# Kernel tuning notes

Measured on AMD Instinct MI355X. Metric: run time of the kernel, lower is better.

## Reference

```python
import jax, jax.numpy as jnp
import numpy as np

C = 256; GC = 32; G = C // GC; K = 3; S = 1; NEW = 2; PAD = (K - 1) // 2
IN1 = C * K * 2 + C * K * K // 32          # 1608
OUT1 = G * NEW * NEW * K * K // 4          # 72
OUT2 = G * NEW * NEW * K * K               # 288
B = 8; H = 56; W = 56


def setup_inputs():
    key = jax.random.key(0)
    k0, k1, k2 = jax.random.split(key, 3)
    inputs = jax.random.normal(k0, (B, C, H, W), jnp.float32)
    W1 = jax.random.normal(k1, (OUT1, IN1), jnp.float32) * np.float32(1.0 / np.sqrt(IN1))
    b1 = jnp.zeros((OUT1,), jnp.float32)
    W2 = jax.random.normal(k2, (OUT2, OUT1), jnp.float32) * np.float32(1.0 / np.sqrt(OUT1))
    b2 = jnp.zeros((OUT2,), jnp.float32)
    return {"inputs": inputs, "W1": W1, "b1": b1, "W2": W2, "b2": b2}


def _unfold(x, h, w):
    # torch.nn.Unfold(K, 1, PAD, S): patches of shape (B, C, K, K, h, w)
    xp = jnp.pad(x, ((0, 0), (0, 0), (PAD, PAD), (PAD, PAD)))
    cols = [xp[:, :, di:di + (h - 1) * S + 1:S, dj:dj + (w - 1) * S + 1:S]
            for di in range(K) for dj in range(K)]  # fixed K*K=9 slices
    return jnp.stack(cols, axis=2).reshape(x.shape[0], x.shape[1], K, K, h, w)


def reference(inputs, W1, b1, W2, b2):
    b, c, Hh, Ww = inputs.shape
    h = (Hh + 2 * PAD - K) // S + 1
    w = (Ww + 2 * PAD - K) // S + 1
    # (B, G, GC, K, K, h, w)
    x = _unfold(inputs, h, w).reshape(b, G, GC, K, K, h, w)
    # three max-pooled descriptors over different axes
    x1 = x.reshape(b, G, -1, GC // 32, K, K, h, w).max(axis=2).reshape(b, -1, h, w)  # (B, C*K*K//32, h, w)
    x2 = x.max(axis=3).reshape(b, -1, h, w)  # (B, C*K, h, w)
    x3 = x.max(axis=4).reshape(b, -1, h, w)  # (B, C*K, h, w)
    feat = jnp.concatenate([x1, x2, x3], axis=1)  # (B, IN1, h, w)
    # two biased 1x1 convs (ConvModule with no norm/act)
    y = jnp.einsum('bchw,oc->bohw', feat, W1) + b1[None, :, None, None]
    y = jnp.einsum('bchw,oc->bohw', y, W2) + b2[None, :, None, None]
    # softmax over the K*K kernel-window dim
    wgt = jax.nn.softmax(y.reshape(b, G, K * K, NEW * NEW, h, w), axis=2)
    # softmax-weighted local aggregation: sum over kernel window
    agg = jnp.einsum('bgckhw,bgknhw->bgcnhw', x.reshape(b, G, GC, K * K, h, w), wgt)
    # fold with non-overlapping (NEW, NEW) blocks == block upsampling reshape
    return agg.reshape(b, C, NEW, NEW, h, w).transpose(0, 1, 4, 2, 5, 3).reshape(b, C, h * NEW, w * NEW)
```

## Files before the change

kernel.cpp:

```cpp
#include <hip/hip_runtime.h>

#define CC   256
#define HH   56
#define WWID 56
#define KIN1 1608
#define KP1  1632
#define NO1  72
#define NO2  288
#define PPB  14
#define H2   112
#define W2D  112

typedef unsigned short u16;
typedef unsigned int   u32;
typedef __attribute__((ext_vector_type(8))) short v8s;
typedef __attribute__((ext_vector_type(4))) float v4f;
typedef __attribute__((ext_vector_type(4))) unsigned short us4;

#define W1BF_ELEMS (80 * KP1)
#define W2BF_OFF_B 262144

#define LDS_TOTAL 35840
#define OFF_A 0
#define OFF_B 21504
#define OFF_C 29696
#define OFF_D 32768

#define SWZ(row) (((row) & 7) << 3)

__device__ __forceinline__ u16 f2b(float x) {
  u32 u = __float_as_uint(x);
  u = (u + 0x7FFFu + ((u >> 16) & 1u)) >> 16;
  return (u16)u;
}

__global__ void kConvW(const float* __restrict__ W1, const float* __restrict__ W2,
                       u16* __restrict__ w1bf, u16* __restrict__ w2bf) {
  int idx = blockIdx.x * 256 + threadIdx.x;
  if (idx < W1BF_ELEMS) {
    int m = idx / KP1, k = idx - m * KP1;
    float v = 0.f;
    if (m < NO1) {
      int orig = -1;
      if (k < 768)                 orig = 72 + (k & 255) * 3 + (k >> 8);
      else if (k < 1536)           orig = 840 + (k & 255) * 3 + ((k - 768) >> 8);
      else if ((k - 1536) < NO1)   orig = k - 1536;
      if (orig >= 0) v = W1[m * KIN1 + orig];
    }
    w1bf[idx] = f2b(v);
  } else {
    int i2 = idx - W1BF_ELEMS;
    if (i2 < NO2 * 96) {
      int m = i2 / 96, k = i2 - m * 96;
      w2bf[i2] = (k < NO1) ? f2b(W2[m * NO1 + k]) : (u16)0;
    }
  }
}

__global__ __launch_bounds__(256, 4)
void kFused(const float* __restrict__ in, const u16* __restrict__ w1bf,
            const float* __restrict__ b1, const u16* __restrict__ w2bf,
            const float* __restrict__ b2, float* __restrict__ out) {
  __shared__ __align__(16) char lds[LDS_TOTAL];
  u16*   rowmaxT = (u16*)(lds + OFF_A);
  u16*   colmaxT = (u16*)(lds + OFF_B);
  u16*   x1T     = (u16*)(lds + OFF_C);
  u16*   y1b     = (u16*)(lds + OFF_D);
  float* y2L     = (float*)(lds + OFF_A);

  const int t  = threadIdx.x;
  const int L  = blockIdx.x + 4 * (blockIdx.y + 56 * blockIdx.z);
  const int jq = L >> 3;
  const int jt = jq & 3, i = jq >> 2, b = L & 7;
  const int c  = t;
  const int g  = c >> 5;
  const int gc = c & 31;
  const int w  = t >> 6, lane = t & 63;
  const int ml = lane & 15, quad = lane >> 4;

  {
    u32* xu = (u32*)x1T;
    u32* yu = (u32*)y1b;
    if (t < 132) {
#pragma unroll
      for (int rp2 = 0; rp2 < 2; ++rp2) {
        int idx = 2 * t + rp2;
        int off;
        if (idx < 192) {
          int row = idx / 12;
          off = (row * 48 + 36 + (idx - row * 12)) ^ ((row & 7) << 2);
        } else {
          int e = idx - 192, row = 14 + e / 36;
          off = (row * 48 + (e % 36)) ^ ((row & 7) << 2);
        }
        xu[off] = 0u;
        yu[off] = 0u;
      }
    }
  }

  const float* rowbase0 = in + ((size_t)b * CC + c) * (HH * WWID);
  u32 win_p[3][8];
  float colmax[16];
#pragma unroll
  for (int k = 0; k < 16; ++k) colmax[k] = -3.0e38f;

#pragma unroll
  for (int r = 0; r < 3; ++r) {
    const int row = i - 1 + r;
    float sc[16];
    if (row < 0 || row >= HH) {
#pragma unroll
      for (int k = 0; k < 16; ++k) sc[k] = 0.f;
    } else {
      const float* rp = rowbase0 + row * WWID;
      float l[20];
      if (jt == 0) {
        const float4 a0 = *(const float4*)(rp), a1 = *(const float4*)(rp + 4),
                     a2 = *(const float4*)(rp + 8), a3 = *(const float4*)(rp + 12);
        l[0]=a0.x;l[1]=a0.y;l[2]=a0.z;l[3]=a0.w; l[4]=a1.x;l[5]=a1.y;l[6]=a1.z;l[7]=a1.w;
        l[8]=a2.x;l[9]=a2.y;l[10]=a2.z;l[11]=a2.w; l[12]=a3.x;l[13]=a3.y;l[14]=a3.z;l[15]=a3.w;
        sc[0] = 0.f;
#pragma unroll
        for (int k = 1; k < 16; ++k) sc[k] = l[k - 1];
      } else if (jt == 3) {
        const float* q = rp + 40;
        const float4 a0 = *(const float4*)(q), a1 = *(const float4*)(q + 4),
                     a2 = *(const float4*)(q + 8), a3 = *(const float4*)(q + 12);
        l[0]=a0.x;l[1]=a0.y;l[2]=a0.z;l[3]=a0.w; l[4]=a1.x;l[5]=a1.y;l[6]=a1.z;l[7]=a1.w;
        l[8]=a2.x;l[9]=a2.y;l[10]=a2.z;l[11]=a2.w; l[12]=a3.x;l[13]=a3.y;l[14]=a3.z;l[15]=a3.w;
#pragma unroll
        for (int k = 0; k < 15; ++k) sc[k] = l[k + 1];
        sc[15] = 0.f;
      } else {
        const float* q = rp + ((jt == 1) ? 12 : 24);
        const float4 a0 = *(const float4*)(q), a1 = *(const float4*)(q + 4),
                     a2 = *(const float4*)(q + 8), a3 = *(const float4*)(q + 12),
                     a4 = *(const float4*)(q + 16);
        l[0]=a0.x;l[1]=a0.y;l[2]=a0.z;l[3]=a0.w; l[4]=a1.x;l[5]=a1.y;l[6]=a1.z;l[7]=a1.w;
        l[8]=a2.x;l[9]=a2.y;l[10]=a2.z;l[11]=a2.w; l[12]=a3.x;l[13]=a3.y;l[14]=a3.z;l[15]=a3.w;
        l[16]=a4.x;l[17]=a4.y;l[18]=a4.z;l[19]=a4.w;
        if (jt == 1) {
#pragma unroll
          for (int k = 0; k < 16; ++k) sc[k] = l[k + 1];
        } else {
#pragma unroll
          for (int k = 0; k < 16; ++k) sc[k] = l[k + 3];
        }
      }
    }
#pragma unroll
    for (int k = 0; k < 16; ++k) colmax[k] = fmaxf(colmax[k], sc[k]);
#pragma unroll
    for (int n = 0; n < 14; ++n)
      rowmaxT[(n * 768 + r * 256 + c) ^ SWZ(n)] =
          f2b(fmaxf(fmaxf(sc[n], sc[n + 1]), sc[n + 2]));
#pragma unroll
    for (int col = 0; col < 16; ++col) {
      float m = sc[col];
      m = fmaxf(m, __shfl_xor(m, 1));
      m = fmaxf(m, __shfl_xor(m, 2));
      m = fmaxf(m, __shfl_xor(m, 4));
      m = fmaxf(m, __shfl_xor(m, 8));
      m = fmaxf(m, __shfl_xor(m, 16));
      if (gc == col) {
        u16 mv = f2b(m);
#pragma unroll
        for (int kj = 0; kj < 3; ++kj) {
          const int n = col - kj;
          if (n >= 0 && n < 14)
            x1T[(n * 96 + g * 9 + r * 3 + kj) ^ SWZ(n)] = mv;
        }
      }
    }
#pragma unroll
    for (int k = 0; k < 8; ++k)
      win_p[r][k] = (u32)f2b(sc[2 * k]) | ((u32)f2b(sc[2 * k + 1]) << 16);
  }
#pragma unroll
  for (int col = 0; col < 16; ++col)
    colmaxT[(col * 256 + c) ^ SWZ(col)] = f2b(colmax[col]);
  __syncthreads();

  auto loadB = [&](int ks) -> v8s {
    if (ks < 24) {
      int kj = ks >> 3, c0 = (ks & 7) * 32, rowi = ml + kj;
      return *(v8s*)&colmaxT[(rowi * 256 + c0 + quad * 8) ^ SWZ(rowi)];
    } else if (ks < 48) {
      return *(v8s*)&rowmaxT[(ml * 768 + (ks - 24) * 32 + quad * 8) ^ SWZ(ml)];
    } else {
      return *(v8s*)&x1T[(ml * 96 + (ks - 48) * 32 + quad * 8) ^ SWZ(ml)];
    }
  };

  {
    v4f acc0 = (v4f){0.f, 0.f, 0.f, 0.f};
    const u16* ap0 = w1bf + (w * 16 + ml) * KP1 + quad * 8;
    if (w == 0) {
      v4f acc1 = (v4f){0.f, 0.f, 0.f, 0.f};
      const u16* ap1 = w1bf + (64 + ml) * KP1 + quad * 8;
#pragma unroll
      for (int ks = 0; ks < 51; ++ks) {
        v8s bf = loadB(ks);
        v8s a0 = *(const v8s*)(ap0 + ks * 32);
        v8s a1 = *(const v8s*)(ap1 + ks * 32);
        acc0 = __builtin_amdgcn_mfma_f32_16x16x32_bf16(a0, bf, acc0, 0, 0, 0);
        acc1 = __builtin_amdgcn_mfma_f32_16x16x32_bf16(a1, bf, acc1, 0, 0, 0);
      }
      if (ml < 14) {
        const float4 bv0 = *(const float4*)(b1 + quad * 4);
        us4 h0;
        h0.x = f2b(acc0[0] + bv0.x); h0.y = f2b(acc0[1] + bv0.y);
        h0.z = f2b(acc0[2] + bv0.z); h0.w = f2b(acc0[3] + bv0.w);
        *(us4*)&y1b[(ml * 96 + quad * 4) ^ SWZ(ml)] = h0;
        if (quad < 2) {
          const float4 bv1 = *(const float4*)(b1 + 64 + quad * 4);
          us4 h1;
          h1.x = f2b(acc1[0] + bv1.x); h1.y = f2b(acc1[1] + bv1.y);
          h1.z = f2b(acc1[2] + bv1.z); h1.w = f2b(acc1[3] + bv1.w);
          *(us4*)&y1b[(ml * 96 + 64 + quad * 4) ^ SWZ(ml)] = h1;
        }
      }
    } else {
#pragma unroll
      for (int ks = 0; ks < 51; ++ks) {
        v8s bf = loadB(ks);
        v8s a0 = *(const v8s*)(ap0 + ks * 32);
        acc0 = __builtin_amdgcn_mfma_f32_16x16x32_bf16(a0, bf, acc0, 0, 0, 0);
      }
      if (ml < 14) {
        const float4 bv0 = *(const float4*)(b1 + w * 16 + quad * 4);
        us4 h0;
        h0.x = f2b(acc0[0] + bv0.x); h0.y = f2b(acc0[1] + bv0.y);
        h0.z = f2b(acc0[2] + bv0.z); h0.w = f2b(acc0[3] + bv0.w);
        *(us4*)&y1b[(ml * 96 + w * 16 + quad * 4) ^ SWZ(ml)] = h0;
      }
    }
  }
  __syncthreads();

  {
    v8s bfr[3];
#pragma unroll
    for (int ks = 0; ks < 3; ++ks)
      bfr[ks] = *(v8s*)&y1b[(ml * 96 + ks * 32 + quad * 8) ^ SWZ(ml)];
    const int mt0 = (w < 2) ? 5 * w : 10 + 4 * (w - 2);
    const int mtn = (w < 2) ? 5 : 4;
    for (int mi = 0; mi < mtn; ++mi) {
      const int mt = mt0 + mi;
      v4f a2 = (v4f){0.f, 0.f, 0.f, 0.f};
#pragma unroll
      for (int ks = 0; ks < 3; ++ks) {
        v8s af = *(const v8s*)&w2bf[(mt * 16 + ml) * 96 + ks * 32 + quad * 8];
        a2 = __builtin_amdgcn_mfma_f32_16x16x32_bf16(af, bfr[ks], a2, 0, 0, 0);
      }
      const int o0 = mt * 16 + quad * 4;
      const float4 bv = *(const float4*)(b2 + o0);
      a2[0] += bv.x; a2[1] += bv.y; a2[2] += bv.z; a2[3] += bv.w;
      *(v4f*)&y2L[ml * 296 + o0] = a2;
    }
  }
  __syncthreads();

#pragma unroll
  for (int it = 0; it < 2; ++it) {
    int s2 = t + it * 256;
    if (s2 < 448) {
      int gg = s2 / 56, rem = s2 - gg * 56, nn = rem / PPB, n = rem - nn * PPB;
      float* bp = &y2L[n * 296 + gg * 36 + nn];
      float v9[9], m = -1e30f;
#pragma unroll
      for (int k = 0; k < 9; ++k) { v9[k] = bp[k * 4]; m = fmaxf(m, v9[k]); }
      float sum = 0.f;
#pragma unroll
      for (int k = 0; k < 9; ++k) { v9[k] = __expf(v9[k] - m); sum += v9[k]; }
      float inv = 1.f / sum;
#pragma unroll
      for (int k = 0; k < 9; ++k) bp[k * 4] = v9[k] * inv;
    }
  }
  __syncthreads();

  {
    float* orow0 = out + ((size_t)(b * CC + c) * H2 + (size_t)(2 * i)) * W2D + 28 * jt;
    float* orow1 = orow0 + W2D;
#pragma unroll
    for (int x = 0; x < 7; ++x) {
      const v4f* wp0 = (const v4f*)&y2L[(2 * x) * 296 + g * 36];
      const v4f* wp1 = (const v4f*)&y2L[(2 * x + 1) * 296 + g * 36];
      float e0 = 0.f, e1 = 0.f, e2 = 0.f, e3 = 0.f;
      float o0 = 0.f, o1 = 0.f, o2 = 0.f, o3 = 0.f;
#pragma unroll
      for (int r = 0; r < 3; ++r) {
        u32 ua = win_p[r][x], ub = win_p[r][x + 1];
        float ex0 = __uint_as_float(ua << 16);
        float ex1 = __uint_as_float(ua & 0xffff0000u);
        float ex2 = __uint_as_float(ub << 16);
        float ox2 = __uint_as_float(ub & 0xffff0000u);
#pragma unroll
        for (int kj = 0; kj < 3; ++kj) {
          v4f wv0 = wp0[r * 3 + kj];
          v4f wv1 = wp1[r * 3 + kj];
          float xe = (kj == 0) ? ex0 : (kj == 1) ? ex1 : ex2;
          float xo = (kj == 0) ? ex1 : (kj == 1) ? ex2 : ox2;
          e0 = fmaf(xe, wv0[0], e0); e1 = fmaf(xe, wv0[1], e1);
          e2 = fmaf(xe, wv0[2], e2); e3 = fmaf(xe, wv0[3], e3);
          o0 = fmaf(xo, wv1[0], o0); o1 = fmaf(xo, wv1[1], o1);
          o2 = fmaf(xo, wv1[2], o2); o3 = fmaf(xo, wv1[3], o3);
        }
      }
      v4f v0 = (v4f){e0, e1, o0, o1};
      v4f v1 = (v4f){e2, e3, o2, o3};
      *(v4f*)(orow0 + 4 * x) = v0;
      *(v4f*)(orow1 + 4 * x) = v1;
    }
  }
}

extern "C" void kernel_launch(void* const* d_in, const int* in_sizes, int n_in,
                              void* d_out, int out_size, void* d_ws, size_t ws_size,
                              hipStream_t stream) {
  const float* in = (const float*)d_in[0];
  const float* W1 = (const float*)d_in[1];
  const float* b1 = (const float*)d_in[2];
  const float* W2 = (const float*)d_in[3];
  const float* b2 = (const float*)d_in[4];
  float* out = (float*)d_out;

  u16* w1bf = (u16*)d_ws;
  u16* w2bf = (u16*)((char*)d_ws + W2BF_OFF_B);

  const int B = in_sizes[0] / (CC * HH * WWID);

  kConvW<<<dim3((W1BF_ELEMS + NO2 * 96 + 255) / 256), 256, 0, stream>>>(W1, W2, w1bf, w2bf);
  dim3 grid(WWID / PPB, HH, B);
  kFused<<<grid, 256, 0, stream>>>(in, w1bf, b1, w2bf, b2, out);
}
```

Baseline: 215.6 us.

## Split fifth W1 output tile across all waves with LDS partial-sum reduction

```diff
diff --git a/kernel.cpp b/kernel.cpp
--- a/kernel.cpp
+++ b/kernel.cpp
@@ -20,11 +20,14 @@
 #define W1BF_ELEMS (80 * KP1)
 #define W2BF_OFF_B 262144
 
-#define LDS_TOTAL 35840
+#define LDS_TOTAL 39936
 #define OFF_A 0
 #define OFF_B 21504
 #define OFF_C 29696
 #define OFF_D 32768
+#define OFF_E 35840
+
+#define Y2S 300
 
 #define SWZ(row) (((row) & 7) << 3)
 
@@ -66,6 +69,7 @@
   u16*   colmaxT = (u16*)(lds + OFF_B);
   u16*   x1T     = (u16*)(lds + OFF_C);
   u16*   y1b     = (u16*)(lds + OFF_D);
+  float* partE   = (float*)(lds + OFF_E);
   float* y2L     = (float*)(lds + OFF_A);
 
   const int t  = threadIdx.x;
@@ -195,47 +199,38 @@
 
   {
     v4f acc0 = (v4f){0.f, 0.f, 0.f, 0.f};
+    v4f acc4 = (v4f){0.f, 0.f, 0.f, 0.f};
+    const int ks0 = w * 13, ks1 = (w == 3) ? 51 : ks0 + 13;
     const u16* ap0 = w1bf + (w * 16 + ml) * KP1 + quad * 8;
-    if (w == 0) {
-      v4f acc1 = (v4f){0.f, 0.f, 0.f, 0.f};
-      const u16* ap1 = w1bf + (64 + ml) * KP1 + quad * 8;
-#pragma unroll
-      for (int ks = 0; ks < 51; ++ks) {
-        v8s bf = loadB(ks);
-        v8s a0 = *(const v8s*)(ap0 + ks * 32);
-        v8s a1 = *(const v8s*)(ap1 + ks * 32);
-        acc0 = __builtin_amdgcn_mfma_f32_16x16x32_bf16(a0, bf, acc0, 0, 0, 0);
-        acc1 = __builtin_amdgcn_mfma_f32_16x16x32_bf16(a1, bf, acc1, 0, 0, 0);
-      }
-      if (ml < 14) {
-        const float4 bv0 = *(const float4*)(b1 + quad * 4);
-        us4 h0;
-        h0.x = f2b(acc0[0] + bv0.x); h0.y = f2b(acc0[1] + bv0.y);
-        h0.z = f2b(acc0[2] + bv0.z); h0.w = f2b(acc0[3] + bv0.w);
-        *(us4*)&y1b[(ml * 96 + quad * 4) ^ SWZ(ml)] = h0;
-        if (quad < 2) {
-          const float4 bv1 = *(const float4*)(b1 + 64 + quad * 4);
-          us4 h1;
-          h1.x = f2b(acc1[0] + bv1.x); h1.y = f2b(acc1[1] + bv1.y);
-          h1.z = f2b(acc1[2] + bv1.z); h1.w = f2b(acc1[3] + bv1.w);
-          *(us4*)&y1b[(ml * 96 + 64 + quad * 4) ^ SWZ(ml)] = h1;
-        }
-      }
-    } else {
-#pragma unroll
-      for (int ks = 0; ks < 51; ++ks) {
-        v8s bf = loadB(ks);
-        v8s a0 = *(const v8s*)(ap0 + ks * 32);
-        acc0 = __builtin_amdgcn_mfma_f32_16x16x32_bf16(a0, bf, acc0, 0, 0, 0);
-      }
-      if (ml < 14) {
-        const float4 bv0 = *(const float4*)(b1 + w * 16 + quad * 4);
-        us4 h0;
-        h0.x = f2b(acc0[0] + bv0.x); h0.y = f2b(acc0[1] + bv0.y);
-        h0.z = f2b(acc0[2] + bv0.z); h0.w = f2b(acc0[3] + bv0.w);
-        *(us4*)&y1b[(ml * 96 + w * 16 + quad * 4) ^ SWZ(ml)] = h0;
-      }
-    }
+    const u16* ap4 = w1bf + (64 + ml) * KP1 + quad * 8;
+#pragma unroll
+    for (int ks = 0; ks < 51; ++ks) {
+      v8s bf = loadB(ks);
+      v8s a0 = *(const v8s*)(ap0 + ks * 32);
+      acc0 = __builtin_amdgcn_mfma_f32_16x16x32_bf16(a0, bf, acc0, 0, 0, 0);
+      if (ks >= ks0 && ks < ks1) {
+        v8s a4 = *(const v8s*)(ap4 + ks * 32);
+        acc4 = __builtin_amdgcn_mfma_f32_16x16x32_bf16(a4, bf, acc4, 0, 0, 0);
+      }
+    }
+    *(v4f*)&partE[((w * 16 + ml) * 16) + quad * 4] = acc4;
+    if (ml < 14) {
+      const float4 bv0 = *(const float4*)(b1 + w * 16 + quad * 4);
+      us4 h0;
+      h0.x = f2b(acc0[0] + bv0.x); h0.y = f2b(acc0[1] + bv0.y);
+      h0.z = f2b(acc0[2] + bv0.z); h0.w = f2b(acc0[3] + bv0.w);
+      *(us4*)&y1b[(ml * 96 + w * 16 + quad * 4) ^ SWZ(ml)] = h0;
+    }
+  }
+  __syncthreads();
+
+  if (t < 112) {
+    const int n = t >> 3, mp = t & 7;
+    float s = b1[64 + mp];
+#pragma unroll
+    for (int ww = 0; ww < 4; ++ww)
+      s += partE[((ww * 16 + n) * 16) + mp];
+    y1b[(n * 96 + 64 + mp) ^ SWZ(n)] = f2b(s);
   }
   __syncthreads();
 
@@ -257,7 +252,7 @@
       const int o0 = mt * 16 + quad * 4;
       const float4 bv = *(const float4*)(b2 + o0);
       a2[0] += bv.x; a2[1] += bv.y; a2[2] += bv.z; a2[3] += bv.w;
-      *(v4f*)&y2L[ml * 296 + o0] = a2;
+      *(v4f*)&y2L[ml * Y2S + o0] = a2;
     }
   }
   __syncthreads();
@@ -267,7 +262,7 @@
     int s2 = t + it * 256;
     if (s2 < 448) {
       int gg = s2 / 56, rem = s2 - gg * 56, nn = rem / PPB, n = rem - nn * PPB;
-      float* bp = &y2L[n * 296 + gg * 36 + nn];
+      float* bp = &y2L[n * Y2S + gg * 36 + nn];
       float v9[9], m = -1e30f;
 #pragma unroll
       for (int k = 0; k < 9; ++k) { v9[k] = bp[k * 4]; m = fmaxf(m, v9[k]); }
@@ -286,8 +281,8 @@
     float* orow1 = orow0 + W2D;
 #pragma unroll
     for (int x = 0; x < 7; ++x) {
-      const v4f* wp0 = (const v4f*)&y2L[(2 * x) * 296 + g * 36];
-      const v4f* wp1 = (const v4f*)&y2L[(2 * x + 1) * 296 + g * 36];
+      const v4f* wp0 = (const v4f*)&y2L[(2 * x) * Y2S + g * 36];
+      const v4f* wp1 = (const v4f*)&y2L[(2 * x + 1) * Y2S + g * 36];
       float e0 = 0.f, e1 = 0.f, e2 = 0.f, e3 = 0.f;
       float o0 = 0.f, o1 = 0.f, o2 = 0.f, o3 = 0.f;
 #pragma unroll
```

Result: slower. 221.0 us (+2.5%).
